# Kernel tuning notes

Hardware: AMD Instinct MI355X
Metric: run time of the kernel (lower is better)

Reference implementation:

```python
import jax, jax.numpy as jnp
import numpy as np

N_NODES = 50000
N_EDGES = 800000
IN_FEATS, H_FEATS, N_CLASSES = 64, 64, 16


def setup_inputs() -> dict:
    key = jax.random.key(0)
    ks = jax.random.split(key, 8)
    x = jax.random.normal(ks[0], (N_NODES, IN_FEATS), dtype=jnp.float32)
    src = jax.random.randint(ks[1], (N_EDGES,), 0, N_NODES, dtype=jnp.int64)
    dst = jax.random.randint(ks[2], (N_EDGES,), 0, N_NODES, dtype=jnp.int64)
    W_self1 = jax.random.normal(ks[3], (IN_FEATS, H_FEATS), dtype=jnp.float32) / np.sqrt(IN_FEATS)
    W_neigh1 = jax.random.normal(ks[4], (IN_FEATS, H_FEATS), dtype=jnp.float32) / np.sqrt(IN_FEATS)
    b1 = jnp.zeros((H_FEATS,), dtype=jnp.float32)
    W_self2 = jax.random.normal(ks[5], (H_FEATS, N_CLASSES), dtype=jnp.float32) / np.sqrt(H_FEATS)
    W_neigh2 = jax.random.normal(ks[6], (H_FEATS, N_CLASSES), dtype=jnp.float32) / np.sqrt(H_FEATS)
    b2 = jnp.zeros((N_CLASSES,), dtype=jnp.float32)
    return {"x": x, "src": src, "dst": dst,
            "W_self1": W_self1, "W_neigh1": W_neigh1, "b1": b1,
            "W_self2": W_self2, "W_neigh2": W_neigh2, "b2": b2}


def _mean_agg(h, src, dst, n_nodes):
    # gather source-node features along edges, sum into destinations, divide by in-degree
    summed = jax.ops.segment_sum(h[src], dst, num_segments=n_nodes)  # [N, d]
    deg = jax.ops.segment_sum(jnp.ones_like(src, dtype=h.dtype), dst, num_segments=n_nodes)
    return summed / jnp.maximum(deg, 1.0)[:, None]  # zero in-degree -> zeros (DGL semantics)


def _sage_layer(h, src, dst, W_self, W_neigh, b):
    h_neigh = _mean_agg(h, src, dst, h.shape[0])
    return h @ W_self + h_neigh @ W_neigh + b


def reference(x, src, dst, W_self1, W_neigh1, b1, W_self2, W_neigh2, b2):
    h = _sage_layer(x, src, dst, W_self1, W_neigh1, b1)
    h = jax.nn.relu(h)
    out = _sage_layer(h, src, dst, W_self2, W_neigh2, b2)
    return out
```

## Files before the change

kernel.cpp:

```cpp
#include <hip/hip_runtime.h>
#include <hip/hip_bf16.h>
#include <cstring>


#define FEATS 64
#define CLS   16
#define EPT   8
#define CAP   5120

typedef unsigned short bf16_t;

__device__ __forceinline__ float bfbits2f(unsigned lo16) {
    unsigned v = lo16 << 16;
    float f;
    __builtin_memcpy(&f, &v, 4);
    return f;
}
__device__ __forceinline__ bf16_t f2bf(float f) {
    unsigned u;
    __builtin_memcpy(&u, &f, 4);
    u = (u + 0x7FFFu + ((u >> 16) & 1u)) >> 16;
    return (bf16_t)u;
}
__device__ __forceinline__ unsigned pack2(float a, float b) {
    return (unsigned)f2bf(a) | ((unsigned)f2bf(b) << 16);
}

__global__ __launch_bounds__(256) void partition_kernel(const int* __restrict__ src,
                                                        const int* __restrict__ dst,
                                                        int* __restrict__ bucket_cnt,
                                                        int* __restrict__ epart, int E) {
    __shared__ int hist[256];
    __shared__ int base[256];
    int t = threadIdx.x;
    int e0 = blockIdx.x * (256 * EPT);
    hist[t] = 0;
    __syncthreads();
    int pk[EPT];
    int bk[EPT];
#pragma unroll
    for (int j = 0; j < EPT; ++j) {
        int e = e0 + j * 256 + t;
        if (e < E) {
            int d = dst[e];
            pk[j] = (src[e] << 8) | (d & 255);
            bk[j] = d >> 8;
            atomicAdd(&hist[bk[j]], 1);
        } else bk[j] = -1;
    }
    __syncthreads();
    int c = hist[t];
    if (c) base[t] = atomicAdd(&bucket_cnt[t], c);
    hist[t] = 0;
    __syncthreads();
#pragma unroll
    for (int j = 0; j < EPT; ++j) {
        if (bk[j] >= 0) {
            int r = atomicAdd(&hist[bk[j]], 1);
            epart[bk[j] * CAP + base[bk[j]] + r] = pk[j];
        }
    }
}

__global__ __launch_bounds__(256) void buildcsr_kernel(const int* __restrict__ epart,
                                                       const int* __restrict__ bucket_cnt,
                                                       int* __restrict__ row_start,
                                                       unsigned short* __restrict__ deg16,
                                                       int* __restrict__ csr, int N) {
    __shared__ int cnt[256];
    __shared__ int pref[256];
    __shared__ int s[256];
    int t = threadIdx.x;
    int b = blockIdx.x;
    int ebeg = b * CAP;
    int ecnt = bucket_cnt[b];
    cnt[t] = 0;
    __syncthreads();
    for (int e = t; e < ecnt; e += 256)
        atomicAdd(&cnt[epart[ebeg + e] & 255], 1);
    __syncthreads();
    int v = cnt[t];
    s[t] = v;
    __syncthreads();
    for (int off = 1; off < 256; off <<= 1) {
        int u = (t >= off) ? s[t - off] : 0;
        __syncthreads();
        s[t] += u;
        __syncthreads();
    }
    pref[t] = s[t] - v;
    int node = b * 256 + t;
    if (node < N) {
        row_start[node] = ebeg + pref[t];
        deg16[node] = (unsigned short)v;
    }
    cnt[t] = 0;
    __syncthreads();
    for (int e = t; e < ecnt; e += 256) {
        int pk = epart[ebeg + e];
        int ln = pk & 255;
        int r = atomicAdd(&cnt[ln], 1);
        csr[ebeg + pref[ln] + r] = pk >> 8;
    }
}

__global__ __launch_bounds__(256) void gemm1_kernel(
    const float* __restrict__ x, const float* __restrict__ Ws,
    const float* __restrict__ Wn, float* __restrict__ selfo,
    bf16_t* __restrict__ t1, int N)
{
    __shared__ float Wc[64 * 128];
    __shared__ float xs[128 * 65];
    int t = threadIdx.x;
    int node0 = blockIdx.x * 128;

    for (int idx = t; idx < 64 * 128; idx += 256) {
        int k = idx >> 7, c = idx & 127;
        Wc[idx] = (c < 64) ? Ws[k * 64 + c] : Wn[k * 64 + (c - 64)];
    }
    for (int idx = t; idx < 128 * 16; idx += 256) {
        int row = idx >> 4, c4 = idx & 15;
        int node = node0 + row;
        float4 v = (node < N) ? ((const float4*)(x + (size_t)node * 64))[c4]
                              : make_float4(0.f, 0.f, 0.f, 0.f);
        float* p = &xs[row * 65 + c4 * 4];
        p[0] = v.x; p[1] = v.y; p[2] = v.z; p[3] = v.w;
    }
    __syncthreads();

    int m = t & 31;
    int g = t >> 5;
    float acc[4][16];
#pragma unroll
    for (int j = 0; j < 4; ++j)
#pragma unroll
        for (int c = 0; c < 16; ++c) acc[j][c] = 0.f;

    for (int k = 0; k < 64; ++k) {
        float w[16];
        const float* wp = &Wc[k * 128 + g * 16];
#pragma unroll
        for (int c = 0; c < 16; ++c) w[c] = wp[c];
        float a0 = xs[m * 65 + k];
        float a1 = xs[(m + 32) * 65 + k];
        float a2 = xs[(m + 64) * 65 + k];
        float a3 = xs[(m + 96) * 65 + k];
#pragma unroll
        for (int c = 0; c < 16; ++c) {
            acc[0][c] += a0 * w[c];
            acc[1][c] += a1 * w[c];
            acc[2][c] += a2 * w[c];
            acc[3][c] += a3 * w[c];
        }
    }
#pragma unroll
    for (int j = 0; j < 4; ++j) {
        int node = node0 + m + 32 * j;
        if (node < N) {
            if (g < 4) {
                float* dstp = selfo + (size_t)node * 64 + g * 16;
#pragma unroll
                for (int c = 0; c < 16; c += 4)
                    *(float4*)(dstp + c) = make_float4(acc[j][c], acc[j][c + 1],
                                                       acc[j][c + 2], acc[j][c + 3]);
            } else {
                bf16_t* dstp = t1 + (size_t)node * 64 + (g - 4) * 16;
                uint4 p0, p1;
                p0.x = pack2(acc[j][0],  acc[j][1]);  p0.y = pack2(acc[j][2],  acc[j][3]);
                p0.z = pack2(acc[j][4],  acc[j][5]);  p0.w = pack2(acc[j][6],  acc[j][7]);
                p1.x = pack2(acc[j][8],  acc[j][9]);  p1.y = pack2(acc[j][10], acc[j][11]);
                p1.z = pack2(acc[j][12], acc[j][13]); p1.w = pack2(acc[j][14], acc[j][15]);
                *(uint4*)(dstp) = p0;
                *(uint4*)(dstp + 8) = p1;
            }
        }
    }
}

__global__ __launch_bounds__(256) void gather64_kernel(
    const int* __restrict__ csr, const int* __restrict__ row_start,
    const unsigned short* __restrict__ deg16,
    const bf16_t* __restrict__ t1, const float* __restrict__ selfo,
    bf16_t* __restrict__ h1, const float* __restrict__ b1, int N)
{
    int wid = (blockIdx.x * 256 + threadIdx.x) >> 6;
    int lane = threadIdx.x & 63;
    int eslot = lane >> 4;
    int cg = lane & 15;
    if (wid >= N) return;
    int beg = row_start[wid];
    int d = deg16[wid];
    float ax = 0.f, ay = 0.f, az = 0.f, aw = 0.f;
    int i = eslot;
    for (; i + 12 < d; i += 16) {
        int s0 = csr[beg + i];
        int s1 = csr[beg + i + 4];
        int s2 = csr[beg + i + 8];
        int s3 = csr[beg + i + 12];
        uint2 r0 = *(const uint2*)(t1 + (size_t)s0 * 64 + cg * 4);
        uint2 r1 = *(const uint2*)(t1 + (size_t)s1 * 64 + cg * 4);
        uint2 r2 = *(const uint2*)(t1 + (size_t)s2 * 64 + cg * 4);
        uint2 r3 = *(const uint2*)(t1 + (size_t)s3 * 64 + cg * 4);
        ax += bfbits2f(r0.x & 0xffff) + bfbits2f(r1.x & 0xffff)
            + bfbits2f(r2.x & 0xffff) + bfbits2f(r3.x & 0xffff);
        ay += bfbits2f(r0.x >> 16) + bfbits2f(r1.x >> 16)
            + bfbits2f(r2.x >> 16) + bfbits2f(r3.x >> 16);
        az += bfbits2f(r0.y & 0xffff) + bfbits2f(r1.y & 0xffff)
            + bfbits2f(r2.y & 0xffff) + bfbits2f(r3.y & 0xffff);
        aw += bfbits2f(r0.y >> 16) + bfbits2f(r1.y >> 16)
            + bfbits2f(r2.y >> 16) + bfbits2f(r3.y >> 16);
    }
    for (; i < d; i += 4) {
        int s0 = csr[beg + i];
        uint2 r0 = *(const uint2*)(t1 + (size_t)s0 * 64 + cg * 4);
        ax += bfbits2f(r0.x & 0xffff);
        ay += bfbits2f(r0.x >> 16);
        az += bfbits2f(r0.y & 0xffff);
        aw += bfbits2f(r0.y >> 16);
    }
    ax += __shfl_xor(ax, 16); ay += __shfl_xor(ay, 16);
    az += __shfl_xor(az, 16); aw += __shfl_xor(aw, 16);
    ax += __shfl_xor(ax, 32); ay += __shfl_xor(ay, 32);
    az += __shfl_xor(az, 32); aw += __shfl_xor(aw, 32);
    if (eslot == 0) {
        float inv = 1.f / fmaxf((float)d, 1.f);
        size_t o = (size_t)wid * 64 + cg * 4;
        float4 s4 = *(const float4*)(selfo + o);
        float4 bb = *(const float4*)(b1 + cg * 4);
        float rx = fmaxf(s4.x + ax * inv + bb.x, 0.f);
        float ry = fmaxf(s4.y + ay * inv + bb.y, 0.f);
        float rz = fmaxf(s4.z + az * inv + bb.z, 0.f);
        float rw = fmaxf(s4.w + aw * inv + bb.w, 0.f);
        uint2 pk;
        pk.x = pack2(rx, ry);
        pk.y = pack2(rz, rw);
        *(uint2*)(h1 + o) = pk;
    }
}

__global__ __launch_bounds__(256) void gemm2_kernel(
    const bf16_t* __restrict__ h1, const float* __restrict__ Ws,
    const float* __restrict__ Wn, float* __restrict__ outp,
    bf16_t* __restrict__ t2, int N)
{
    __shared__ float Wc[64 * 32];
    __shared__ float xs[128 * 65];
    int t = threadIdx.x;
    int node0 = blockIdx.x * 128;

    for (int idx = t; idx < 64 * 32; idx += 256) {
        int k = idx >> 5, c = idx & 31;
        Wc[idx] = (c < 16) ? Ws[k * 16 + c] : Wn[k * 16 + (c - 16)];
    }
    for (int idx = t; idx < 128 * 8; idx += 256) {
        int row = idx >> 3, c8 = idx & 7;
        int node = node0 + row;
        float* p = &xs[row * 65 + c8 * 8];
        if (node < N) {
            uint4 u = *(const uint4*)(h1 + (size_t)node * 64 + c8 * 8);
            p[0] = bfbits2f(u.x & 0xffff); p[1] = bfbits2f(u.x >> 16);
            p[2] = bfbits2f(u.y & 0xffff); p[3] = bfbits2f(u.y >> 16);
            p[4] = bfbits2f(u.z & 0xffff); p[5] = bfbits2f(u.z >> 16);
            p[6] = bfbits2f(u.w & 0xffff); p[7] = bfbits2f(u.w >> 16);
        } else {
            for (int q = 0; q < 8; ++q) p[q] = 0.f;
        }
    }
    __syncthreads();

    int m = t & 31;
    int g = t >> 5;
    float acc[4][4];
#pragma unroll
    for (int j = 0; j < 4; ++j)
#pragma unroll
        for (int c = 0; c < 4; ++c) acc[j][c] = 0.f;

    for (int k = 0; k < 64; ++k) {
        float w[4];
        const float* wp = &Wc[k * 32 + g * 4];
#pragma unroll
        for (int c = 0; c < 4; ++c) w[c] = wp[c];
        float a0 = xs[m * 65 + k];
        float a1 = xs[(m + 32) * 65 + k];
        float a2 = xs[(m + 64) * 65 + k];
        float a3 = xs[(m + 96) * 65 + k];
#pragma unroll
        for (int c = 0; c < 4; ++c) {
            acc[0][c] += a0 * w[c];
            acc[1][c] += a1 * w[c];
            acc[2][c] += a2 * w[c];
            acc[3][c] += a3 * w[c];
        }
    }
#pragma unroll
    for (int j = 0; j < 4; ++j) {
        int node = node0 + m + 32 * j;
        if (node < N) {
            if (g < 4) {
                *(float4*)(outp + (size_t)node * 16 + g * 4) =
                    make_float4(acc[j][0], acc[j][1], acc[j][2], acc[j][3]);
            } else {
                uint2 pk;
                pk.x = pack2(acc[j][0], acc[j][1]);
                pk.y = pack2(acc[j][2], acc[j][3]);
                *(uint2*)(t2 + (size_t)node * 16 + (g - 4) * 4) = pk;
            }
        }
    }
}

__global__ __launch_bounds__(256) void gather16_kernel(
    const int* __restrict__ csr, const int* __restrict__ row_start,
    const unsigned short* __restrict__ deg16,
    const bf16_t* __restrict__ t2,
    float* __restrict__ outp, const float* __restrict__ b2, int N)
{
    int gt = blockIdx.x * 256 + threadIdx.x;
    int node = gt >> 3;
    int c2 = gt & 7;
    if (node >= N) return;
    int beg = row_start[node];
    int d = deg16[node];
    int end = beg + d;
    float a0 = 0.f, a1 = 0.f;
    int i = beg;
    for (; i + 4 <= end; i += 4) {
        int s0 = csr[i], s1 = csr[i + 1], s2 = csr[i + 2], s3 = csr[i + 3];
        unsigned u0 = *(const unsigned*)(t2 + (size_t)s0 * 16 + c2 * 2);
        unsigned u1 = *(const unsigned*)(t2 + (size_t)s1 * 16 + c2 * 2);
        unsigned u2 = *(const unsigned*)(t2 + (size_t)s2 * 16 + c2 * 2);
        unsigned u3 = *(const unsigned*)(t2 + (size_t)s3 * 16 + c2 * 2);
        a0 += bfbits2f(u0 & 0xffff) + bfbits2f(u1 & 0xffff)
            + bfbits2f(u2 & 0xffff) + bfbits2f(u3 & 0xffff);
        a1 += bfbits2f(u0 >> 16) + bfbits2f(u1 >> 16)
            + bfbits2f(u2 >> 16) + bfbits2f(u3 >> 16);
    }
    for (; i < end; ++i) {
        int s = csr[i];
        unsigned u = *(const unsigned*)(t2 + (size_t)s * 16 + c2 * 2);
        a0 += bfbits2f(u & 0xffff);
        a1 += bfbits2f(u >> 16);
    }
    float inv = 1.f / fmaxf((float)d, 1.f);
    size_t o = (size_t)node * 16 + c2 * 2;
    outp[o]     += a0 * inv + b2[c2 * 2];
    outp[o + 1] += a1 * inv + b2[c2 * 2 + 1];
}

extern "C" void kernel_launch(void* const* d_in, const int* in_sizes, int n_in,
                              void* d_out, int out_size, void* d_ws, size_t ws_size,
                              hipStream_t stream) {
    const float* x   = (const float*)d_in[0];
    const int*   src = (const int*)d_in[1];
    const int*   dst = (const int*)d_in[2];
    const float* Ws1 = (const float*)d_in[3];
    const float* Wn1 = (const float*)d_in[4];
    const float* b1  = (const float*)d_in[5];
    const float* Ws2 = (const float*)d_in[6];
    const float* Wn2 = (const float*)d_in[7];
    const float* b2  = (const float*)d_in[8];
    float* outp = (float*)d_out;

    const int N = in_sizes[0] / FEATS;
    const int E = in_sizes[1];
    const int B = (N + 255) / 256;

    char* p = (char*)d_ws;
    auto align16 = [](char* q) { return (char*)(((size_t)q + 15) & ~(size_t)15); };
    int* bucket_cnt    = (int*)p;                  p = (char*)(bucket_cnt + 256);
    int* epart         = (int*)p;                  p = (char*)(epart + (size_t)B * CAP);
    int* csr           = (int*)p;                  p = (char*)(csr + (size_t)B * CAP);
    int* row_start     = (int*)align16(p);         p = (char*)(row_start + N);
    unsigned short* deg16 = (unsigned short*)align16(p); p = (char*)(deg16 + N);
    float* selfo       = (float*)align16(p);       p = (char*)(selfo + (size_t)N * 64);
    bf16_t* t1         = (bf16_t*)align16(p);      p = (char*)(t1 + (size_t)N * 64);
    bf16_t* h1         = (bf16_t*)align16(p);      p = (char*)(h1 + (size_t)N * 64);
    bf16_t* t2         = (bf16_t*)align16(p);

    hipMemsetAsync(bucket_cnt, 0, 256 * sizeof(int), stream);

    partition_kernel<<<(E + 256 * EPT - 1) / (256 * EPT), 256, 0, stream>>>(
        src, dst, bucket_cnt, epart, E);
    buildcsr_kernel<<<B, 256, 0, stream>>>(epart, bucket_cnt, row_start, deg16, csr, N);

    gemm1_kernel<<<(N + 127) / 128, 256, 0, stream>>>(x, Ws1, Wn1, selfo, t1, N);
    gather64_kernel<<<((size_t)N * 64 + 255) / 256, 256, 0, stream>>>(
        csr, row_start, deg16, t1, selfo, h1, b1, N);
    gemm2_kernel<<<(N + 127) / 128, 256, 0, stream>>>(h1, Ws2, Wn2, outp, t2, N);
    gather16_kernel<<<((size_t)N * 8 + 255) / 256, 256, 0, stream>>>(
        csr, row_start, deg16, t2, outp, b2, N);
}
```

Measured before the change: 170.4 us.

## Replace CSR build and per-node gathers with bucketed LDS atomic aggregation

Drops the CSR construction kernel and aggregates neighbor features straight from the per-bucket edge partition. Each 512-thread block accumulates its 256 destination nodes in shared memory with float atomics and also counts in-degree there. The self-term output of gemm1 is now stored in bf16 to cut memory traffic, and the partition kernel handles 16 edges per thread. The trade is heavy LDS atomic contention, a large shared-memory footprint per block (about 66KB for agg64) that limits occupancy, and only 196 blocks, in exchange for one fewer kernel and no CSR writes and reads.

```diff
diff --git a/kernel.cpp b/kernel.cpp
--- a/kernel.cpp
+++ b/kernel.cpp
@@ -5,7 +5,7 @@
 
 #define FEATS 64
 #define CLS   16
-#define EPT   8
+#define EPT   16
 #define CAP   5120
 
 typedef unsigned short bf16_t;
@@ -24,6 +24,16 @@
 }
 __device__ __forceinline__ unsigned pack2(float a, float b) {
     return (unsigned)f2bf(a) | ((unsigned)f2bf(b) << 16);
+}
+__device__ __forceinline__ void acc8(float* ap, uint4 r) {
+    atomicAdd(ap + 0, bfbits2f(r.x & 0xffff));
+    atomicAdd(ap + 1, bfbits2f(r.x >> 16));
+    atomicAdd(ap + 2, bfbits2f(r.y & 0xffff));
+    atomicAdd(ap + 3, bfbits2f(r.y >> 16));
+    atomicAdd(ap + 4, bfbits2f(r.z & 0xffff));
+    atomicAdd(ap + 5, bfbits2f(r.z >> 16));
+    atomicAdd(ap + 6, bfbits2f(r.w & 0xffff));
+    atomicAdd(ap + 7, bfbits2f(r.w >> 16));
 }
 
 __global__ __launch_bounds__(256) void partition_kernel(const int* __restrict__ src,
@@ -62,51 +72,9 @@
     }
 }
 
-__global__ __launch_bounds__(256) void buildcsr_kernel(const int* __restrict__ epart,
-                                                       const int* __restrict__ bucket_cnt,
-                                                       int* __restrict__ row_start,
-                                                       unsigned short* __restrict__ deg16,
-                                                       int* __restrict__ csr, int N) {
-    __shared__ int cnt[256];
-    __shared__ int pref[256];
-    __shared__ int s[256];
-    int t = threadIdx.x;
-    int b = blockIdx.x;
-    int ebeg = b * CAP;
-    int ecnt = bucket_cnt[b];
-    cnt[t] = 0;
-    __syncthreads();
-    for (int e = t; e < ecnt; e += 256)
-        atomicAdd(&cnt[epart[ebeg + e] & 255], 1);
-    __syncthreads();
-    int v = cnt[t];
-    s[t] = v;
-    __syncthreads();
-    for (int off = 1; off < 256; off <<= 1) {
-        int u = (t >= off) ? s[t - off] : 0;
-        __syncthreads();
-        s[t] += u;
-        __syncthreads();
-    }
-    pref[t] = s[t] - v;
-    int node = b * 256 + t;
-    if (node < N) {
-        row_start[node] = ebeg + pref[t];
-        deg16[node] = (unsigned short)v;
-    }
-    cnt[t] = 0;
-    __syncthreads();
-    for (int e = t; e < ecnt; e += 256) {
-        int pk = epart[ebeg + e];
-        int ln = pk & 255;
-        int r = atomicAdd(&cnt[ln], 1);
-        csr[ebeg + pref[ln] + r] = pk >> 8;
-    }
-}
-
 __global__ __launch_bounds__(256) void gemm1_kernel(
     const float* __restrict__ x, const float* __restrict__ Ws,
-    const float* __restrict__ Wn, float* __restrict__ selfo,
+    const float* __restrict__ Wn, bf16_t* __restrict__ selfo,
     bf16_t* __restrict__ t1, int N)
 {
     __shared__ float Wc[64 * 128];
@@ -157,84 +125,73 @@
     for (int j = 0; j < 4; ++j) {
         int node = node0 + m + 32 * j;
         if (node < N) {
-            if (g < 4) {
-                float* dstp = selfo + (size_t)node * 64 + g * 16;
-#pragma unroll
-                for (int c = 0; c < 16; c += 4)
-                    *(float4*)(dstp + c) = make_float4(acc[j][c], acc[j][c + 1],
-                                                       acc[j][c + 2], acc[j][c + 3]);
-            } else {
-                bf16_t* dstp = t1 + (size_t)node * 64 + (g - 4) * 16;
-                uint4 p0, p1;
-                p0.x = pack2(acc[j][0],  acc[j][1]);  p0.y = pack2(acc[j][2],  acc[j][3]);
-                p0.z = pack2(acc[j][4],  acc[j][5]);  p0.w = pack2(acc[j][6],  acc[j][7]);
-                p1.x = pack2(acc[j][8],  acc[j][9]);  p1.y = pack2(acc[j][10], acc[j][11]);
-                p1.z = pack2(acc[j][12], acc[j][13]); p1.w = pack2(acc[j][14], acc[j][15]);
-                *(uint4*)(dstp) = p0;
-                *(uint4*)(dstp + 8) = p1;
-            }
-        }
-    }
-}
-
-__global__ __launch_bounds__(256) void gather64_kernel(
-    const int* __restrict__ csr, const int* __restrict__ row_start,
-    const unsigned short* __restrict__ deg16,
-    const bf16_t* __restrict__ t1, const float* __restrict__ selfo,
-    bf16_t* __restrict__ h1, const float* __restrict__ b1, int N)
+            bf16_t* dstp = ((g < 4) ? selfo : t1) + (size_t)node * 64 + (g & 3) * 16;
+            uint4 p0, p1;
+            p0.x = pack2(acc[j][0],  acc[j][1]);  p0.y = pack2(acc[j][2],  acc[j][3]);
+            p0.z = pack2(acc[j][4],  acc[j][5]);  p0.w = pack2(acc[j][6],  acc[j][7]);
+            p1.x = pack2(acc[j][8],  acc[j][9]);  p1.y = pack2(acc[j][10], acc[j][11]);
+            p1.z = pack2(acc[j][12], acc[j][13]); p1.w = pack2(acc[j][14], acc[j][15]);
+            *(uint4*)(dstp) = p0;
+            *(uint4*)(dstp + 8) = p1;
+        }
+    }
+}
+
+__global__ __launch_bounds__(512) void agg64_kernel(
+    const int* __restrict__ epart, const int* __restrict__ bucket_cnt,
+    const bf16_t* __restrict__ t1, const bf16_t* __restrict__ selfo,
+    const float* __restrict__ b1, bf16_t* __restrict__ h1, int N)
 {
-    int wid = (blockIdx.x * 256 + threadIdx.x) >> 6;
-    int lane = threadIdx.x & 63;
-    int eslot = lane >> 4;
-    int cg = lane & 15;
-    if (wid >= N) return;
-    int beg = row_start[wid];
-    int d = deg16[wid];
-    float ax = 0.f, ay = 0.f, az = 0.f, aw = 0.f;
-    int i = eslot;
-    for (; i + 12 < d; i += 16) {
-        int s0 = csr[beg + i];
-        int s1 = csr[beg + i + 4];
-        int s2 = csr[beg + i + 8];
-        int s3 = csr[beg + i + 12];
-        uint2 r0 = *(const uint2*)(t1 + (size_t)s0 * 64 + cg * 4);
-        uint2 r1 = *(const uint2*)(t1 + (size_t)s1 * 64 + cg * 4);
-        uint2 r2 = *(const uint2*)(t1 + (size_t)s2 * 64 + cg * 4);
-        uint2 r3 = *(const uint2*)(t1 + (size_t)s3 * 64 + cg * 4);
-        ax += bfbits2f(r0.x & 0xffff) + bfbits2f(r1.x & 0xffff)
-            + bfbits2f(r2.x & 0xffff) + bfbits2f(r3.x & 0xffff);
-        ay += bfbits2f(r0.x >> 16) + bfbits2f(r1.x >> 16)
-            + bfbits2f(r2.x >> 16) + bfbits2f(r3.x >> 16);
-        az += bfbits2f(r0.y & 0xffff) + bfbits2f(r1.y & 0xffff)
-            + bfbits2f(r2.y & 0xffff) + bfbits2f(r3.y & 0xffff);
-        aw += bfbits2f(r0.y >> 16) + bfbits2f(r1.y >> 16)
-            + bfbits2f(r2.y >> 16) + bfbits2f(r3.y >> 16);
-    }
-    for (; i < d; i += 4) {
-        int s0 = csr[beg + i];
-        uint2 r0 = *(const uint2*)(t1 + (size_t)s0 * 64 + cg * 4);
-        ax += bfbits2f(r0.x & 0xffff);
-        ay += bfbits2f(r0.x >> 16);
-        az += bfbits2f(r0.y & 0xffff);
-        aw += bfbits2f(r0.y >> 16);
-    }
-    ax += __shfl_xor(ax, 16); ay += __shfl_xor(ay, 16);
-    az += __shfl_xor(az, 16); aw += __shfl_xor(aw, 16);
-    ax += __shfl_xor(ax, 32); ay += __shfl_xor(ay, 32);
-    az += __shfl_xor(az, 32); aw += __shfl_xor(aw, 32);
-    if (eslot == 0) {
-        float inv = 1.f / fmaxf((float)d, 1.f);
-        size_t o = (size_t)wid * 64 + cg * 4;
-        float4 s4 = *(const float4*)(selfo + o);
-        float4 bb = *(const float4*)(b1 + cg * 4);
-        float rx = fmaxf(s4.x + ax * inv + bb.x, 0.f);
-        float ry = fmaxf(s4.y + ay * inv + bb.y, 0.f);
-        float rz = fmaxf(s4.z + az * inv + bb.z, 0.f);
-        float rw = fmaxf(s4.w + aw * inv + bb.w, 0.f);
-        uint2 pk;
-        pk.x = pack2(rx, ry);
-        pk.y = pack2(rz, rw);
-        *(uint2*)(h1 + o) = pk;
+    __shared__ float acc[256 * 65];
+    int t = threadIdx.x;
+    int b = blockIdx.x;
+    for (int idx = t; idx < 256 * 65; idx += 512) acc[idx] = 0.f;
+    __syncthreads();
+
+    int ecnt = bucket_cnt[b];
+    int ebeg = b * CAP;
+    int sub = t >> 3;
+    int q = t & 7;
+    int e = sub;
+    for (; e + 64 < ecnt; e += 128) {
+        int pk0 = epart[ebeg + e];
+        int pk1 = epart[ebeg + e + 64];
+        uint4 r0 = *(const uint4*)(t1 + (size_t)(pk0 >> 8) * 64 + q * 8);
+        uint4 r1 = *(const uint4*)(t1 + (size_t)(pk1 >> 8) * 64 + q * 8);
+        int ln0 = pk0 & 255, ln1 = pk1 & 255;
+        acc8(&acc[ln0 * 65 + q * 8], r0);
+        acc8(&acc[ln1 * 65 + q * 8], r1);
+        if (q == 0) {
+            atomicAdd(&acc[ln0 * 65 + 64], 1.0f);
+            atomicAdd(&acc[ln1 * 65 + 64], 1.0f);
+        }
+    }
+    for (; e < ecnt; e += 64) {
+        int pk0 = epart[ebeg + e];
+        uint4 r0 = *(const uint4*)(t1 + (size_t)(pk0 >> 8) * 64 + q * 8);
+        int ln0 = pk0 & 255;
+        acc8(&acc[ln0 * 65 + q * 8], r0);
+        if (q == 0) atomicAdd(&acc[ln0 * 65 + 64], 1.0f);
+    }
+    __syncthreads();
+
+    for (int idx = t; idx < 256 * 16; idx += 512) {
+        int ln = idx >> 4, c4 = idx & 15;
+        int node = b * 256 + ln;
+        if (node < N) {
+            float inv = 1.f / fmaxf(acc[ln * 65 + 64], 1.f);
+            uint2 su = *(const uint2*)(selfo + (size_t)node * 64 + c4 * 4);
+            float4 bb = *(const float4*)(b1 + c4 * 4);
+            const float* ap = &acc[ln * 65 + c4 * 4];
+            float rx = fmaxf(bfbits2f(su.x & 0xffff) + ap[0] * inv + bb.x, 0.f);
+            float ry = fmaxf(bfbits2f(su.x >> 16)    + ap[1] * inv + bb.y, 0.f);
+            float rz = fmaxf(bfbits2f(su.y & 0xffff) + ap[2] * inv + bb.z, 0.f);
+            float rw = fmaxf(bfbits2f(su.y >> 16)    + ap[3] * inv + bb.w, 0.f);
+            uint2 pk2;
+            pk2.x = pack2(rx, ry);
+            pk2.y = pack2(rz, rw);
+            *(uint2*)(h1 + (size_t)node * 64 + c4 * 4) = pk2;
+        }
     }
 }
 
@@ -263,7 +220,7 @@
             p[4] = bfbits2f(u.z & 0xffff); p[5] = bfbits2f(u.z >> 16);
             p[6] = bfbits2f(u.w & 0xffff); p[7] = bfbits2f(u.w >> 16);
         } else {
-            for (int q = 0; q < 8; ++q) p[q] = 0.f;
+            for (int qq = 0; qq < 8; ++qq) p[qq] = 0.f;
         }
     }
     __syncthreads();
@@ -310,42 +267,59 @@
     }
 }
 
-__global__ __launch_bounds__(256) void gather16_kernel(
-    const int* __restrict__ csr, const int* __restrict__ row_start,
-    const unsigned short* __restrict__ deg16,
-    const bf16_t* __restrict__ t2,
-    float* __restrict__ outp, const float* __restrict__ b2, int N)
+__global__ __launch_bounds__(512) void agg16_kernel(
+    const int* __restrict__ epart, const int* __restrict__ bucket_cnt,
+    const bf16_t* __restrict__ t2, const float* __restrict__ b2,
+    float* __restrict__ outp, int N)
 {
-    int gt = blockIdx.x * 256 + threadIdx.x;
-    int node = gt >> 3;
-    int c2 = gt & 7;
-    if (node >= N) return;
-    int beg = row_start[node];
-    int d = deg16[node];
-    int end = beg + d;
-    float a0 = 0.f, a1 = 0.f;
-    int i = beg;
-    for (; i + 4 <= end; i += 4) {
-        int s0 = csr[i], s1 = csr[i + 1], s2 = csr[i + 2], s3 = csr[i + 3];
-        unsigned u0 = *(const unsigned*)(t2 + (size_t)s0 * 16 + c2 * 2);
-        unsigned u1 = *(const unsigned*)(t2 + (size_t)s1 * 16 + c2 * 2);
-        unsigned u2 = *(const unsigned*)(t2 + (size_t)s2 * 16 + c2 * 2);
-        unsigned u3 = *(const unsigned*)(t2 + (size_t)s3 * 16 + c2 * 2);
-        a0 += bfbits2f(u0 & 0xffff) + bfbits2f(u1 & 0xffff)
-            + bfbits2f(u2 & 0xffff) + bfbits2f(u3 & 0xffff);
-        a1 += bfbits2f(u0 >> 16) + bfbits2f(u1 >> 16)
-            + bfbits2f(u2 >> 16) + bfbits2f(u3 >> 16);
-    }
-    for (; i < end; ++i) {
-        int s = csr[i];
-        unsigned u = *(const unsigned*)(t2 + (size_t)s * 16 + c2 * 2);
-        a0 += bfbits2f(u & 0xffff);
-        a1 += bfbits2f(u >> 16);
-    }
-    float inv = 1.f / fmaxf((float)d, 1.f);
-    size_t o = (size_t)node * 16 + c2 * 2;
-    outp[o]     += a0 * inv + b2[c2 * 2];
-    outp[o + 1] += a1 * inv + b2[c2 * 2 + 1];
+    __shared__ float acc[256 * 17];
+    int t = threadIdx.x;
+    int b = blockIdx.x;
+    for (int idx = t; idx < 256 * 17; idx += 512) acc[idx] = 0.f;
+    __syncthreads();
+
+    int ecnt = bucket_cnt[b];
+    int ebeg = b * CAP;
+    int sub = t >> 1;
+    int q = t & 1;
+    int e = sub;
+    for (; e + 256 < ecnt; e += 512) {
+        int pk0 = epart[ebeg + e];
+        int pk1 = epart[ebeg + e + 256];
+        uint4 r0 = *(const uint4*)(t2 + (size_t)(pk0 >> 8) * 16 + q * 8);
+        uint4 r1 = *(const uint4*)(t2 + (size_t)(pk1 >> 8) * 16 + q * 8);
+        int ln0 = pk0 & 255, ln1 = pk1 & 255;
+        acc8(&acc[ln0 * 17 + q * 8], r0);
+        acc8(&acc[ln1 * 17 + q * 8], r1);
+        if (q == 0) {
+            atomicAdd(&acc[ln0 * 17 + 16], 1.0f);
+            atomicAdd(&acc[ln1 * 17 + 16], 1.0f);
+        }
+    }
+    for (; e < ecnt; e += 256) {
+        int pk0 = epart[ebeg + e];
+        uint4 r0 = *(const uint4*)(t2 + (size_t)(pk0 >> 8) * 16 + q * 8);
+        int ln0 = pk0 & 255;
+        acc8(&acc[ln0 * 17 + q * 8], r0);
+        if (q == 0) atomicAdd(&acc[ln0 * 17 + 16], 1.0f);
+    }
+    __syncthreads();
+
+    for (int idx = t; idx < 256 * 4; idx += 512) {
+        int ln = idx >> 2, c4 = idx & 3;
+        int node = b * 256 + ln;
+        if (node < N) {
+            float inv = 1.f / fmaxf(acc[ln * 17 + 16], 1.f);
+            const float* ap = &acc[ln * 17 + c4 * 4];
+            float4 bb = *(const float4*)(b2 + c4 * 4);
+            float4 o = *(const float4*)(outp + (size_t)node * 16 + c4 * 4);
+            o.x += ap[0] * inv + bb.x;
+            o.y += ap[1] * inv + bb.y;
+            o.z += ap[2] * inv + bb.z;
+            o.w += ap[3] * inv + bb.w;
+            *(float4*)(outp + (size_t)node * 16 + c4 * 4) = o;
+        }
+    }
 }
 
 extern "C" void kernel_launch(void* const* d_in, const int* in_sizes, int n_in,
@@ -368,26 +342,19 @@
 
     char* p = (char*)d_ws;
     auto align16 = [](char* q) { return (char*)(((size_t)q + 15) & ~(size_t)15); };
-    int* bucket_cnt    = (int*)p;                  p = (char*)(bucket_cnt + 256);
-    int* epart         = (int*)p;                  p = (char*)(epart + (size_t)B * CAP);
-    int* csr           = (int*)p;                  p = (char*)(csr + (size_t)B * CAP);
-    int* row_start     = (int*)align16(p);         p = (char*)(row_start + N);
-    unsigned short* deg16 = (unsigned short*)align16(p); p = (char*)(deg16 + N);
-    float* selfo       = (float*)align16(p);       p = (char*)(selfo + (size_t)N * 64);
-    bf16_t* t1         = (bf16_t*)align16(p);      p = (char*)(t1 + (size_t)N * 64);
-    bf16_t* h1         = (bf16_t*)align16(p);      p = (char*)(h1 + (size_t)N * 64);
-    bf16_t* t2         = (bf16_t*)align16(p);
+    int* bucket_cnt = (int*)p;             p = (char*)(bucket_cnt + 256);
+    int* epart      = (int*)p;             p = (char*)(epart + (size_t)B * CAP);
+    bf16_t* selfo   = (bf16_t*)align16(p); p = (char*)(selfo + (size_t)N * 64);
+    bf16_t* t1      = (bf16_t*)align16(p); p = (char*)(t1 + (size_t)N * 64);
+    bf16_t* h1      = (bf16_t*)align16(p); p = (char*)(h1 + (size_t)N * 64);
+    bf16_t* t2      = (bf16_t*)align16(p);
 
     hipMemsetAsync(bucket_cnt, 0, 256 * sizeof(int), stream);
 
     partition_kernel<<<(E + 256 * EPT - 1) / (256 * EPT), 256, 0, stream>>>(
         src, dst, bucket_cnt, epart, E);
-    buildcsr_kernel<<<B, 256, 0, stream>>>(epart, bucket_cnt, row_start, deg16, csr, N);
-
     gemm1_kernel<<<(N + 127) / 128, 256, 0, stream>>>(x, Ws1, Wn1, selfo, t1, N);
-    gather64_kernel<<<((size_t)N * 64 + 255) / 256, 256, 0, stream>>>(
-        csr, row_start, deg16, t1, selfo, h1, b1, N);
+    agg64_kernel<<<B, 512, 0, stream>>>(epart, bucket_cnt, t1, selfo, b1, h1, N);
     gemm2_kernel<<<(N + 127) / 128, 256, 0, stream>>>(h1, Ws2, Wn2, outp, t2, N);
-    gather16_kernel<<<((size_t)N * 8 + 255) / 256, 256, 0, stream>>>(
-        csr, row_start, deg16, t2, outp, b2, N);
-}
+    agg16_kernel<<<B, 512, 0, stream>>>(epart, bucket_cnt, t2, b2, outp, N);
+}
```

After: 571.3 us. +235.2%, slower.
